# Kernel tuning notes

Hardware: AMD Instinct MI355X
Metric: run time of the kernel (lower is better)

## Reference

```python
import jax, jax.numpy as jnp
import numpy as np

HEAD_SIZE = 64
NUM_HEADS = 8
D_IN = 512

def setup_inputs() -> dict:
    key = jax.random.key(0)
    ks = jax.random.split(key, 6)
    B, Nq, Nk = 4, 2048, 2048
    HD = HEAD_SIZE * NUM_HEADS
    q = jax.random.normal(ks[0], (B, Nq, D_IN), dtype=jnp.float32)
    k = jax.random.normal(ks[1], (B, Nk, D_IN), dtype=jnp.float32)
    s = 1.0 / np.sqrt(D_IN)
    Wq = jax.random.normal(ks[2], (D_IN, HD), dtype=jnp.float32) * s
    Wk = jax.random.normal(ks[3], (D_IN, HD), dtype=jnp.float32) * s
    Wv = jax.random.normal(ks[4], (D_IN, HD), dtype=jnp.float32) * s
    Wh = jax.random.normal(ks[5], (HD, HEAD_SIZE), dtype=jnp.float32) * (1.0 / np.sqrt(HD))
    return {"q": q, "k": k, "Wq": Wq, "Wk": Wk, "Wv": Wv, "Wh": Wh}

def reference(q, k, Wq, Wk, Wv, Wh):
    B, Nq, _ = q.shape
    Nk = k.shape[1]
    H, hs = NUM_HEADS, HEAD_SIZE
    # QKV projections (no bias), reshape to [B, H, N, hs]
    q_ = (q @ Wq).reshape(B, Nq, H, hs).transpose(0, 2, 1, 3)
    k_ = (k @ Wk).reshape(B, Nk, H, hs).transpose(0, 2, 1, 3)
    v_ = (k @ Wv).reshape(B, Nk, H, hs).transpose(0, 2, 1, 3)
    scale = 1.0 / jnp.sqrt(jnp.float32(hs))
    score = jnp.einsum('bhqd,bhkd->bhqk', q_, k_) * scale  # [B,H,Nq,Nk]
    attn = jax.nn.softmax(score, axis=-1)
    wv = jnp.einsum('bhqk,bhkd->bhqd', attn, v_)  # [B,H,Nq,hs]
    wv = wv.transpose(0, 2, 1, 3).reshape(B, Nq, H * hs)
    return wv @ Wh  # [B, Nq, hs]
```

## Files before the change

### kernel.cpp

```cpp
#include <hip/hip_runtime.h>
#include <hip/hip_bf16.h>

#define BB   4
#define NQ   2048
#define NKK  2048
#define DIN  512
#define NH   8
#define HS   64
#define HD   512

typedef __hip_bfloat16 bf16;
typedef unsigned short ushort_t;
typedef __attribute__((ext_vector_type(8))) short short8;
typedef __attribute__((ext_vector_type(4))) float f32x4;
typedef __attribute__((ext_vector_type(16))) float f32x16;
typedef __attribute__((ext_vector_type(4))) unsigned u32x4;

__device__ __forceinline__ unsigned short f2bu(float x) {
  bf16 h = __float2bfloat16(x);
  return *(unsigned short*)&h;
}

__global__ __launch_bounds__(256) void wtrans_kernel(
    const float* __restrict__ Wq, const float* __restrict__ Wk,
    const float* __restrict__ Wv, const float* __restrict__ Wh,
    ushort_t* __restrict__ Wt, ushort_t* __restrict__ Wht) {
  const int z = blockIdx.z;
  const float* src;
  ushort_t* dst;
  int S;
  if (z < 3) {
    src = (z == 0) ? Wq : (z == 1) ? Wk : Wv;
    dst = Wt + (size_t)z * 512 * 512;
    S = 512;
  } else {
    if (blockIdx.y != 0) return;
    src = Wh;
    dst = Wht;
    S = 64;
  }
  const int k0 = blockIdx.x * 64;
  const int n0 = (z < 3) ? blockIdx.y * 64 : 0;

  __shared__ ushort_t Ls[64 * 72];
  const int tid = threadIdx.x;
  {
    int r = tid >> 2, cb = (tid & 3) * 16;
    const float* sp = src + (size_t)(k0 + r) * S + n0 + cb;
#pragma unroll
    for (int ii = 0; ii < 4; ++ii) {
      float4 f = *(const float4*)(sp + ii * 4);
      __align__(8) ushort_t t4[4] = {f2bu(f.x), f2bu(f.y), f2bu(f.z), f2bu(f.w)};
      *(uint2*)(&Ls[r * 72 + cb + ii * 4]) = *(uint2*)t4;
    }
  }
  __syncthreads();
  {
    int rr = tid >> 2, tb = (tid & 3) * 16;
    __align__(16) ushort_t tmp[16];
#pragma unroll
    for (int j = 0; j < 16; ++j) tmp[j] = Ls[(tb + j) * 72 + rr];
    ushort_t* dp = dst + (size_t)(n0 + rr) * 512 + k0 + tb;
    *(int4*)dp       = ((int4*)tmp)[0];
    *(int4*)(dp + 8) = ((int4*)tmp)[1];
  }
}

__global__ __launch_bounds__(256) void proj_kernel(
    const float* __restrict__ q, const float* __restrict__ k,
    const ushort_t* __restrict__ Wt, ushort_t* __restrict__ Qf,
    ushort_t* __restrict__ Kf, ushort_t* __restrict__ Vt) {
  const int z = blockIdx.z;
  const float* X = (z == 0) ? q : k;
  const ushort_t* Wz = Wt + (size_t)z * 512 * 512;
  const float sc = (z == 0) ? 0.18033688011112042f : 1.0f;

  __shared__ ushort_t As[2 * 128 * 40];
  __shared__ ushort_t Bs[2 * 128 * 40];

  const int tid  = threadIdx.x;
  const int lane = tid & 63;
  const int w    = tid >> 6;
  const int quad = lane >> 4;
  const int c    = lane & 15;
  const int wm   = w >> 1, wn = w & 1;

  const int m0 = blockIdx.y * 128;
  const int n0 = blockIdx.x * 128;
  const int sm  = tid >> 1;
  const int skb = (tid & 1) * 16;

  float4 xa[4];
  int4 wb[2];
  auto load_t = [&](int k0) {
    const float* xp = X + (size_t)(m0 + sm) * DIN + k0 + skb;
    xa[0] = *(const float4*)(xp + 0);
    xa[1] = *(const float4*)(xp + 4);
    xa[2] = *(const float4*)(xp + 8);
    xa[3] = *(const float4*)(xp + 12);
    const ushort_t* wp = Wz + (size_t)(n0 + sm) * 512 + k0 + skb;
    wb[0] = *(const int4*)wp;
    wb[1] = *(const int4*)(wp + 8);
  };
  auto store_t = [&](int buf) {
    __align__(16) ushort_t ta[16];
#pragma unroll
    for (int ii = 0; ii < 4; ++ii) {
      ta[ii * 4 + 0] = f2bu(xa[ii].x);
      ta[ii * 4 + 1] = f2bu(xa[ii].y);
      ta[ii * 4 + 2] = f2bu(xa[ii].z);
      ta[ii * 4 + 3] = f2bu(xa[ii].w);
    }
    *(int4*)(&As[buf * 5120 + sm * 40 + skb])     = ((int4*)ta)[0];
    *(int4*)(&As[buf * 5120 + sm * 40 + skb + 8]) = ((int4*)ta)[1];
    *(int4*)(&Bs[buf * 5120 + sm * 40 + skb])     = wb[0];
    *(int4*)(&Bs[buf * 5120 + sm * 40 + skb + 8]) = wb[1];
  };

  f32x4 acc[4][4];
#pragma unroll
  for (int m = 0; m < 4; ++m)
#pragma unroll
    for (int n = 0; n < 4; ++n) acc[m][n] = (f32x4)0.0f;

  load_t(0);
  store_t(0);
  __syncthreads();

  for (int t = 0; t < 16; ++t) {
    const int cur = t & 1;
    if (t < 15) load_t((t + 1) * 32);
    const ushort_t* as = As + cur * 5120;
    const ushort_t* bs = Bs + cur * 5120;
    short8 af[4], bfr[4];
#pragma unroll
    for (int m = 0; m < 4; ++m)
      af[m] = *(const short8*)(&as[(wm * 64 + m * 16 + c) * 40 + quad * 8]);
#pragma unroll
    for (int n = 0; n < 4; ++n)
      bfr[n] = *(const short8*)(&bs[(wn * 64 + n * 16 + c) * 40 + quad * 8]);
#pragma unroll
    for (int m = 0; m < 4; ++m)
#pragma unroll
      for (int n = 0; n < 4; ++n)
        acc[m][n] = __builtin_amdgcn_mfma_f32_16x16x32_bf16(af[m], bfr[n], acc[m][n], 0, 0, 0);
    if (t < 15) store_t(cur ^ 1);
    __syncthreads();
  }

  if (z != 2) {
    ushort_t* Y = (z == 0) ? Qf : Kf;
#pragma unroll
    for (int m = 0; m < 4; ++m)
#pragma unroll
      for (int n = 0; n < 4; ++n)
#pragma unroll
        for (int r = 0; r < 4; ++r) {
          int row = m0 + wm * 64 + m * 16 + quad * 4 + r;
          int col = n0 + wn * 64 + n * 16 + c;
          Y[(size_t)row * HD + col] = f2bu(acc[m][n][r] * sc);
        }
  } else {
#pragma unroll
    for (int m = 0; m < 4; ++m)
#pragma unroll
      for (int n = 0; n < 4; ++n) {
        int row0 = m0 + wm * 64 + m * 16 + quad * 4;
        int col  = n0 + wn * 64 + n * 16 + c;
        int bb   = row0 >> 11;
        int t0   = row0 & 2047;
        __align__(8) ushort_t t4[4] = {f2bu(acc[m][n][0]), f2bu(acc[m][n][1]),
                                       f2bu(acc[m][n][2]), f2bu(acc[m][n][3])};
        *(uint2*)(&Vt[((size_t)bb * HD + col) * NKK + t0]) = *(uint2*)t4;
      }
  }
}

__global__ __launch_bounds__(64, 1) void attn_kernel(
    const ushort_t* __restrict__ Qf, const ushort_t* __restrict__ Kf,
    const ushort_t* __restrict__ Vt, ushort_t* __restrict__ CTX) {
  const int id   = blockIdx.x;
  const int xcd  = id & 7;
  const int slot = id >> 3;
  const int p    = xcd * 4 + (slot >> 5);
  const int qb   = slot & 31;
  const int h    = p & 7;
  const int b    = p >> 3;

  __shared__ ushort_t Kt[2][4096];
  __shared__ ushort_t Vs[2][4096];

  const int lane = threadIdx.x & 63;
  const int ql   = lane & 31;
  const int hi   = lane >> 5;

  const int q0 = qb * 64;

  short8 bq[2][4];
#pragma unroll
  for (int qs = 0; qs < 2; ++qs) {
    const ushort_t* qp =
        Qf + (size_t)(b * NQ + q0 + qs * 32 + ql) * HD + h * HS + hi * 8;
#pragma unroll
    for (int ks = 0; ks < 4; ++ks) bq[qs][ks] = *(const short8*)(qp + ks * 16);
  }

  const int sub  = lane >> 3;
  const int slt  = lane & 7;
  const int csrc = slt ^ sub;
  const ushort_t* kp0 =
      Kf + (size_t)(b * NKK + sub) * HD + h * HS + csrc * 8;
  const ushort_t* vp0 =
      Vt + (size_t)((b * NH + h) * HS + sub) * NKK + csrc * 8;

  auto stage = [&](int buf, int kt) {
    const ushort_t* kp = kp0 + (size_t)kt * 64 * HD;
    const ushort_t* vp = vp0 + (size_t)kt * 64;
#pragma unroll
    for (int i = 0; i < 8; ++i) {
      __builtin_amdgcn_global_load_lds(
          (const __attribute__((address_space(1))) unsigned*)(kp + (size_t)i * 8 * HD),
          (__attribute__((address_space(3))) unsigned*)(&Kt[buf][i * 512]),
          16, 0, 0);
      __builtin_amdgcn_global_load_lds(
          (const __attribute__((address_space(1))) unsigned*)(vp + (size_t)i * 8 * NKK),
          (__attribute__((address_space(3))) unsigned*)(&Vs[buf][i * 512]),
          16, 0, 0);
    }
  };

  f32x16 o[2][2];
#pragma unroll
  for (int qs = 0; qs < 2; ++qs)
#pragma unroll
    for (int ng = 0; ng < 2; ++ng) o[qs][ng] = (f32x16)0.0f;
  float lsum[2] = {0.0f, 0.0f};

  stage(0, 0);

  for (int t = 0; t < NKK / 64; ++t) {
    const int buf = t & 1;
    if (t < NKK / 64 - 1) {
      stage(buf ^ 1, t + 1);
      asm volatile("s_waitcnt vmcnt(16)" ::: "memory");
    } else {
      asm volatile("s_waitcnt vmcnt(0)" ::: "memory");
    }
    const ushort_t* kb = &Kt[buf][0];
    const ushort_t* vb = &Vs[buf][0];

    short8 ak[2][4], bv[2][4];
#pragma unroll
    for (int kg = 0; kg < 2; ++kg) {
      const int krow = kg * 32 + ql;
#pragma unroll
      for (int ks = 0; ks < 4; ++ks)
        ak[kg][ks] = *(const short8*)(&kb[krow * 64 + (((ks * 2 + hi) ^ (krow & 7)) * 8)]);
    }
#pragma unroll
    for (int ng = 0; ng < 2; ++ng) {
      const int vrow = ng * 32 + ql;
#pragma unroll
      for (int ks = 0; ks < 4; ++ks)
        bv[ng][ks] = *(const short8*)(&vb[vrow * 64 + (((ks * 2 + hi) ^ (vrow & 7)) * 8)]);
    }

#pragma unroll
    for (int kg = 0; kg < 2; ++kg) {
      f32x16 s[2];
      s[0] = (f32x16)0.0f;
      s[1] = (f32x16)0.0f;
#pragma unroll
      for (int ks = 0; ks < 4; ++ks) {
        s[0] = __builtin_amdgcn_mfma_f32_32x32x16_bf16(ak[kg][ks], bq[0][ks], s[0], 0, 0, 0);
        s[1] = __builtin_amdgcn_mfma_f32_32x32x16_bf16(ak[kg][ks], bq[1][ks], s[1], 0, 0, 0);
      }

      short8 pa[2][2];
#pragma unroll
      for (int qs = 0; qs < 2; ++qs) {
        float p_[16];
#pragma unroll
        for (int r = 0; r < 16; ++r) p_[r] = __builtin_amdgcn_exp2f(s[qs][r]);
        {
          float a0 = p_[0] + p_[1], a1 = p_[2] + p_[3], a2 = p_[4] + p_[5], a3 = p_[6] + p_[7];
          float a4 = p_[8] + p_[9], a5 = p_[10] + p_[11], a6 = p_[12] + p_[13], a7 = p_[14] + p_[15];
          a0 += a1; a2 += a3; a4 += a5; a6 += a7;
          lsum[qs] += (a0 + a2) + (a4 + a6);
        }
#pragma unroll
        for (int sp = 0; sp < 2; ++sp) {
          unsigned wA, wB, wC, wD;
          asm("v_cvt_pk_bf16_f32 %0, %1, %2" : "=v"(wA) : "v"(p_[8 * sp + 0]), "v"(p_[8 * sp + 1]));
          asm("v_cvt_pk_bf16_f32 %0, %1, %2" : "=v"(wB) : "v"(p_[8 * sp + 2]), "v"(p_[8 * sp + 3]));
          asm("v_cvt_pk_bf16_f32 %0, %1, %2" : "=v"(wC) : "v"(p_[8 * sp + 4]), "v"(p_[8 * sp + 5]));
          asm("v_cvt_pk_bf16_f32 %0, %1, %2" : "=v"(wD) : "v"(p_[8 * sp + 6]), "v"(p_[8 * sp + 7]));
          asm("v_permlane32_swap_b32 %0, %1" : "+v"(wA), "+v"(wC));
          asm("v_permlane32_swap_b32 %0, %1" : "+v"(wB), "+v"(wD));
          u32x4 pw;
          pw.x = wA;
          pw.y = wB;
          pw.z = wC;
          pw.w = wD;
          pa[qs][sp] = __builtin_bit_cast(short8, pw);
        }
      }

#pragma unroll
      for (int sp = 0; sp < 2; ++sp) {
        const int ks = kg * 2 + sp;
#pragma unroll
        for (int ng = 0; ng < 2; ++ng) {
          o[0][ng] = __builtin_amdgcn_mfma_f32_32x32x16_bf16(pa[0][sp], bv[ng][ks], o[0][ng], 0, 0, 0);
          o[1][ng] = __builtin_amdgcn_mfma_f32_32x32x16_bf16(pa[1][sp], bv[ng][ks], o[1][ng], 0, 0, 0);
        }
      }
    }
  }

  float inv[2];
#pragma unroll
  for (int qs = 0; qs < 2; ++qs) {
    float tot = lsum[qs] + __shfl_xor(lsum[qs], 32);
    inv[qs] = 1.0f / tot;
  }

#pragma unroll
  for (int qs = 0; qs < 2; ++qs)
#pragma unroll
    for (int r = 0; r < 16; ++r) {
      int qr = (r & 3) + 8 * (r >> 2) + 4 * hi;
      float iv = __shfl(inv[qs], qr);
      size_t base = (size_t)(b * NQ + q0 + qs * 32 + qr) * HD + h * HS + ql;
      CTX[base]      = f2bu(o[qs][0][r] * iv);
      CTX[base + 32] = f2bu(o[qs][1][r] * iv);
    }
}

__global__ __launch_bounds__(64) void outproj_kernel(
    const ushort_t* __restrict__ CTX, const ushort_t* __restrict__ Wht,
    float* __restrict__ out) {
  const int lane = threadIdx.x & 63;
  const int quad = lane >> 4, c = lane & 15;
  const int m0 = blockIdx.x * 16;

  f32x4 o[4];
#pragma unroll
  for (int n = 0; n < 4; ++n) o[n] = (f32x4)0.0f;

  const ushort_t* arow = CTX + (size_t)(m0 + c) * HD;
#pragma unroll 4
  for (int ks = 0; ks < 16; ++ks) {
    short8 a = *(const short8*)(arow + ks * 32 + quad * 8);
#pragma unroll
    for (int nd = 0; nd < 4; ++nd) {
      short8 bn = *(const short8*)(Wht + (size_t)(nd * 16 + c) * 512 + ks * 32 + quad * 8);
      o[nd] = __builtin_amdgcn_mfma_f32_16x16x32_bf16(a, bn, o[nd], 0, 0, 0);
    }
  }
#pragma unroll
  for (int nd = 0; nd < 4; ++nd)
#pragma unroll
    for (int r = 0; r < 4; ++r)
      out[(size_t)(m0 + quad * 4 + r) * HS + nd * 16 + c] = o[nd][r];
}

extern "C" void kernel_launch(void* const* d_in, const int* in_sizes, int n_in,
                              void* d_out, int out_size, void* d_ws,
                              size_t ws_size, hipStream_t stream) {
  const float* q  = (const float*)d_in[0];
  const float* k  = (const float*)d_in[1];
  const float* Wq = (const float*)d_in[2];
  const float* Wk = (const float*)d_in[3];
  const float* Wv = (const float*)d_in[4];
  const float* Wh = (const float*)d_in[5];
  float* out = (float*)d_out;

  const size_t E = (size_t)BB * NQ * HD;
  ushort_t* ws  = (ushort_t*)d_ws;
  ushort_t* Qf  = ws;
  ushort_t* Kf  = Qf + E;
  ushort_t* Vt  = Kf + E;
  ushort_t* CTX = Vt + E;
  ushort_t* Vf  = CTX + E;
  ushort_t* Wt  = Vf + E;
  ushort_t* Wht = Wt + (size_t)3 * 512 * 512;

  wtrans_kernel<<<dim3(8, 8, 4), 256, 0, stream>>>(Wq, Wk, Wv, Wh, Wt, Wht);
  proj_kernel<<<dim3(HD / 128, BB * NQ / 128, 3), 256, 0, stream>>>(
      q, k, Wt, Qf, Kf, Vt);
  attn_kernel<<<dim3(32 * NH * BB), 64, 0, stream>>>(Qf, Kf, Vt, CTX);
  outproj_kernel<<<dim3(BB * NQ / 16), 64, 0, stream>>>(CTX, Wht, out);
}
```

Baseline: 191.7 us.

## Restructure projection GEMM to stage full 64-row X strip in LDS, stream weights from global

The projection kernel now has each block handle 64 rows across the full 512 output columns. The whole 64x512 input strip is converted to bf16 once and kept in shared memory. Weight fragments are read straight from global memory (L2-resident) instead of through double-buffered LDS tiles, and the inner k-loop has no per-step barriers. Each fp32 input row is read once instead of once per column tile, at the cost of more direct global weight loads, ~65KB LDS per block, a larger accumulator set and fewer blocks (384).

```diff
diff --git a/kernel.cpp b/kernel.cpp
--- a/kernel.cpp
+++ b/kernel.cpp
@@ -70,109 +70,85 @@
     const float* __restrict__ q, const float* __restrict__ k,
     const ushort_t* __restrict__ Wt, ushort_t* __restrict__ Qf,
     ushort_t* __restrict__ Kf, ushort_t* __restrict__ Vt) {
-  const int z = blockIdx.z;
+  const int z = blockIdx.y;
   const float* X = (z == 0) ? q : k;
   const ushort_t* Wz = Wt + (size_t)z * 512 * 512;
   const float sc = (z == 0) ? 0.18033688011112042f : 1.0f;
 
-  __shared__ ushort_t As[2 * 128 * 40];
-  __shared__ ushort_t Bs[2 * 128 * 40];
+  __shared__ ushort_t Xs[64 * 520];
 
   const int tid  = threadIdx.x;
   const int lane = tid & 63;
   const int w    = tid >> 6;
   const int quad = lane >> 4;
   const int c    = lane & 15;
-  const int wm   = w >> 1, wn = w & 1;
-
-  const int m0 = blockIdx.y * 128;
-  const int n0 = blockIdx.x * 128;
-  const int sm  = tid >> 1;
-  const int skb = (tid & 1) * 16;
-
-  float4 xa[4];
-  int4 wb[2];
-  auto load_t = [&](int k0) {
-    const float* xp = X + (size_t)(m0 + sm) * DIN + k0 + skb;
-    xa[0] = *(const float4*)(xp + 0);
-    xa[1] = *(const float4*)(xp + 4);
-    xa[2] = *(const float4*)(xp + 8);
-    xa[3] = *(const float4*)(xp + 12);
-    const ushort_t* wp = Wz + (size_t)(n0 + sm) * 512 + k0 + skb;
-    wb[0] = *(const int4*)wp;
-    wb[1] = *(const int4*)(wp + 8);
-  };
-  auto store_t = [&](int buf) {
-    __align__(16) ushort_t ta[16];
-#pragma unroll
-    for (int ii = 0; ii < 4; ++ii) {
-      ta[ii * 4 + 0] = f2bu(xa[ii].x);
-      ta[ii * 4 + 1] = f2bu(xa[ii].y);
-      ta[ii * 4 + 2] = f2bu(xa[ii].z);
-      ta[ii * 4 + 3] = f2bu(xa[ii].w);
-    }
-    *(int4*)(&As[buf * 5120 + sm * 40 + skb])     = ((int4*)ta)[0];
-    *(int4*)(&As[buf * 5120 + sm * 40 + skb + 8]) = ((int4*)ta)[1];
-    *(int4*)(&Bs[buf * 5120 + sm * 40 + skb])     = wb[0];
-    *(int4*)(&Bs[buf * 5120 + sm * 40 + skb + 8]) = wb[1];
-  };
-
-  f32x4 acc[4][4];
+
+  const int m0 = blockIdx.x * 64;
+
+  {
+    const int r  = tid >> 2;
+    const int c4 = (tid & 3) * 4;
+    const float* xp = X + (size_t)(m0 + r) * DIN;
+    ushort_t* lp = &Xs[r * 520];
+#pragma unroll
+    for (int i = 0; i < 32; ++i) {
+      const int col = c4 + i * 16;
+      float4 f = *(const float4*)(xp + col);
+      __align__(8) ushort_t t4[4] = {f2bu(f.x), f2bu(f.y), f2bu(f.z), f2bu(f.w)};
+      *(uint2*)(lp + col) = *(uint2*)t4;
+    }
+  }
+  __syncthreads();
+
+  const int n0w = w * 128;
+
+  f32x4 acc[4][8];
 #pragma unroll
   for (int m = 0; m < 4; ++m)
 #pragma unroll
-    for (int n = 0; n < 4; ++n) acc[m][n] = (f32x4)0.0f;
-
-  load_t(0);
-  store_t(0);
-  __syncthreads();
-
-  for (int t = 0; t < 16; ++t) {
-    const int cur = t & 1;
-    if (t < 15) load_t((t + 1) * 32);
-    const ushort_t* as = As + cur * 5120;
-    const ushort_t* bs = Bs + cur * 5120;
-    short8 af[4], bfr[4];
+    for (int n = 0; n < 8; ++n) acc[m][n] = (f32x4)0.0f;
+
+#pragma unroll 2
+  for (int ks = 0; ks < 16; ++ks) {
+    short8 af[4];
 #pragma unroll
     for (int m = 0; m < 4; ++m)
-      af[m] = *(const short8*)(&as[(wm * 64 + m * 16 + c) * 40 + quad * 8]);
-#pragma unroll
-    for (int n = 0; n < 4; ++n)
-      bfr[n] = *(const short8*)(&bs[(wn * 64 + n * 16 + c) * 40 + quad * 8]);
+      af[m] = *(const short8*)(&Xs[(m * 16 + c) * 520 + ks * 32 + quad * 8]);
+#pragma unroll
+    for (int n = 0; n < 8; ++n) {
+      short8 bn = *(const short8*)(Wz + (size_t)(n0w + n * 16 + c) * 512 +
+                                   ks * 32 + quad * 8);
+#pragma unroll
+      for (int m = 0; m < 4; ++m)
+        acc[m][n] = __builtin_amdgcn_mfma_f32_16x16x32_bf16(af[m], bn, acc[m][n], 0, 0, 0);
+    }
+  }
+
+  if (z == 2) {
 #pragma unroll
     for (int m = 0; m < 4; ++m)
 #pragma unroll
-      for (int n = 0; n < 4; ++n)
-        acc[m][n] = __builtin_amdgcn_mfma_f32_16x16x32_bf16(af[m], bfr[n], acc[m][n], 0, 0, 0);
-    if (t < 15) store_t(cur ^ 1);
-    __syncthreads();
-  }
-
-  if (z != 2) {
-    ushort_t* Y = (z == 0) ? Qf : Kf;
-#pragma unroll
-    for (int m = 0; m < 4; ++m)
-#pragma unroll
-      for (int n = 0; n < 4; ++n)
-#pragma unroll
-        for (int r = 0; r < 4; ++r) {
-          int row = m0 + wm * 64 + m * 16 + quad * 4 + r;
-          int col = n0 + wn * 64 + n * 16 + c;
-          Y[(size_t)row * HD + col] = f2bu(acc[m][n][r] * sc);
-        }
-  } else {
-#pragma unroll
-    for (int m = 0; m < 4; ++m)
-#pragma unroll
-      for (int n = 0; n < 4; ++n) {
-        int row0 = m0 + wm * 64 + m * 16 + quad * 4;
-        int col  = n0 + wn * 64 + n * 16 + c;
-        int bb   = row0 >> 11;
-        int t0   = row0 & 2047;
+      for (int n = 0; n < 8; ++n) {
+        const int row0 = m0 + m * 16 + quad * 4;
+        const int col  = n0w + n * 16 + c;
+        const int bb   = row0 >> 11;
+        const int t0   = row0 & 2047;
         __align__(8) ushort_t t4[4] = {f2bu(acc[m][n][0]), f2bu(acc[m][n][1]),
                                        f2bu(acc[m][n][2]), f2bu(acc[m][n][3])};
         *(uint2*)(&Vt[((size_t)bb * HD + col) * NKK + t0]) = *(uint2*)t4;
       }
+  } else {
+    ushort_t* Y = (z == 0) ? Qf : Kf;
+#pragma unroll
+    for (int m = 0; m < 4; ++m)
+#pragma unroll
+      for (int n = 0; n < 8; ++n)
+#pragma unroll
+        for (int r = 0; r < 4; ++r) {
+          const int row = m0 + m * 16 + quad * 4 + r;
+          const int col = n0w + n * 16 + c;
+          Y[(size_t)row * HD + col] = f2bu(acc[m][n][r] * sc);
+        }
   }
 }
 
@@ -387,7 +363,7 @@
   ushort_t* Wht = Wt + (size_t)3 * 512 * 512;
 
   wtrans_kernel<<<dim3(8, 8, 4), 256, 0, stream>>>(Wq, Wk, Wv, Wh, Wt, Wht);
-  proj_kernel<<<dim3(HD / 128, BB * NQ / 128, 3), 256, 0, stream>>>(
+  proj_kernel<<<dim3(BB * NQ / 64, 3), 256, 0, stream>>>(
       q, k, Wt, Qf, Kf, Vt);
   attn_kernel<<<dim3(32 * NH * BB), 64, 0, stream>>>(Qf, Kf, Vt, CTX);
   outproj_kernel<<<dim3(BB * NQ / 16), 64, 0, stream>>>(CTX, Wht, out);
```

New measurement: 204.3 us. 1.07x slower.
